# Optimization experiments

Measured on AMD Instinct MI355X. Metric: run time of the kernel, lower is better.

## Reference

```python
import jax, jax.numpy as jnp
import numpy as np

B, S = 32, 1024
ENC_HID, DEC_HID = 512, 512
NEG = -1e10


def setup_inputs() -> dict:
    key = jax.random.key(0)
    k1, k2, k3, k4, k5, k6 = jax.random.split(key, 6)
    hidden = jax.random.normal(k1, (B, DEC_HID), dtype=jnp.float32)
    encoder_outputs = jax.random.normal(k2, (B, S, 2 * ENC_HID), dtype=jnp.float32)
    mask = jax.random.randint(k3, (B, S), 0, 2, dtype=jnp.int32)
    # Linear(enc_hid*2 + dec_hid -> dec_hid): weight [out, in], bias [out]
    in_dim = 2 * ENC_HID + DEC_HID
    W = jax.random.normal(k4, (DEC_HID, in_dim), dtype=jnp.float32) * (1.0 / np.sqrt(in_dim))
    b = jax.random.normal(k5, (DEC_HID,), dtype=jnp.float32) * 0.01
    v = jax.random.uniform(k6, (DEC_HID,), dtype=jnp.float32)  # torch.rand
    return {"hidden": hidden, "encoder_outputs": encoder_outputs, "mask": mask,
            "W": W, "b": b, "v": v}


def reference(hidden, encoder_outputs, mask, W, b, v):
    # cat((hidden_repeated, encoder_outputs)) @ W.T == hidden @ Wh.T + enc @ We.T
    # split W by the concat order: first DEC_HID input cols act on hidden.
    Wh = W[:, :DEC_HID]          # [dec_hid, dec_hid]
    We = W[:, DEC_HID:]          # [dec_hid, 2*enc_hid]
    h_proj = hidden @ Wh.T + b                       # [B, dec_hid]
    e_proj = jnp.einsum('bse,de->bsd', encoder_outputs, We)  # [B, S, dec_hid]
    energy = jnp.tanh(h_proj[:, None, :] + e_proj)   # [B, S, dec_hid]
    scores = energy @ v                               # [B, S]
    scores = jnp.where(mask == 0, NEG, scores)
    return jax.nn.softmax(scores, axis=1)
```

## Files before the change

kernel.cpp:

```cpp
#include <hip/hip_runtime.h>
#include <hip/hip_bf16.h>
#include <math.h>

#define BB 32
#define SS 1024
#define DH 512
#define EH2 1024
#define WROW 1536
#define NEGV -1.0e10f

typedef __attribute__((ext_vector_type(8))) short s16x8;
typedef __attribute__((ext_vector_type(4))) float f32x4;
typedef unsigned short u16;
typedef unsigned int u32;

__device__ __forceinline__ int swzB(int row, int slot) {
    return row * 64 + ((slot ^ (row & 7)) << 3);
}
__device__ __forceinline__ int swzA(int row, int slot) {
    return row * 32 + ((slot ^ ((row >> 1) & 3)) << 3);
}

__device__ __forceinline__ void split8(const float4& v0, const float4& v1,
                                       s16x8& hi, s16x8& lo) {
    float xs[8] = {v0.x, v0.y, v0.z, v0.w, v1.x, v1.y, v1.z, v1.w};
    union { u16 u[8]; s16x8 v; } H, L;
#pragma unroll
    for (int j = 0; j < 8; ++j) {
        u32 u = __builtin_bit_cast(u32, xs[j]);
        u32 hb = u & 0xFFFF0000u;
        float rem = xs[j] - __builtin_bit_cast(float, hb);
        H.u[j] = (u16)(u >> 16);
        L.u[j] = __builtin_bit_cast(u16, __float2bfloat16(rem));
    }
    hi = H.v;
    lo = L.v;
}

__device__ __forceinline__ s16x8 cvt8(const float4& v0, const float4& v1) {
    float xs[8] = {v0.x, v0.y, v0.z, v0.w, v1.x, v1.y, v1.z, v1.w};
    union { u16 u[8]; s16x8 v; } H;
#pragma unroll
    for (int j = 0; j < 8; ++j)
        H.u[j] = __builtin_bit_cast(u16, __float2bfloat16(xs[j]));
    return H.v;
}

__device__ __forceinline__ float fast_tanh(float x) {
    float a = fabsf(x);
    float e = __expf(2.0f * a);
    float r = 1.0f - 2.0f / (e + 1.0f);
    return copysignf(r, x);
}

__global__ void hproj_kernel(const float* __restrict__ hidden,
                             const float* __restrict__ W,
                             const float* __restrict__ bias,
                             float* __restrict__ hproj) {
    int wave = (int)((blockIdx.x * blockDim.x + threadIdx.x) >> 6);
    int lane = threadIdx.x & 63;
    if (wave >= BB * DH) return;
    int b = wave >> 9;
    int d = wave & 511;
    const float* hrow = hidden + b * DH;
    const float* wrow = W + (size_t)d * WROW;
    float sum = 0.f;
#pragma unroll
    for (int u = 0; u < 8; ++u) {
        int k = lane + 64 * u;
        sum = fmaf(hrow[k], wrow[k], sum);
    }
#pragma unroll
    for (int off = 32; off > 0; off >>= 1)
        sum += __shfl_xor(sum, off, 64);
    if (lane == 0) hproj[wave] = sum + bias[d];
}

__global__ void bsplit_kernel(const float* __restrict__ W,
                              u16* __restrict__ img) {
    int idx = blockIdx.x * 256 + threadIdx.x;
    int c = idx >> 7;
    int ko = idx & 127;
    int k = ko * 8;
    const float* src = W + (size_t)c * WROW + DH + k;
    float4 v0 = *(const float4*)src;
    float4 v1 = *(const float4*)(src + 4);
    s16x8 hi, lo;
    split8(v0, v1, hi, lo);
    int nb = c >> 8;
    int cp = c & 255;
    int kt = ko >> 2;
    int sl = ko & 3;
    u16* tb = img + ((size_t)(nb * 32 + kt) << 14);
    *(s16x8*)(tb + swzB(cp, sl)) = hi;
    *(s16x8*)(tb + swzB(cp, sl + 4)) = lo;
}

__global__ __launch_bounds__(512, 4)
void energy_mfma_kernel(const float* __restrict__ enc,
                        const u16* __restrict__ bimg,
                        const float* __restrict__ hproj,
                        const float* __restrict__ v,
                        float* __restrict__ scoresP) {
    __shared__ u16 sA[2][128 * 32];
    __shared__ u16 sB[2][256 * 64];

    const int tid = threadIdx.x;
    const int lane = tid & 63;
    const int wid = tid >> 6;
    const int lr = lane & 15;
    const int lg = lane >> 4;

    const int flat = (blockIdx.x & 7) * 64 + (blockIdx.x >> 3);
    const int nblk = flat & 1;
    const int mblk = flat >> 1;
    const int b = mblk >> 3;
    const int srow = (mblk & 7) * 128;
    const int d0 = nblk * 256;

    const int wm = (wid >> 2) * 64;
    const int wn = (wid & 3) * 64;

    const float* aBase = enc + ((size_t)(b * SS + srow)) * EH2;
    const u16* tBase = bimg + (((size_t)nblk * 32) << 14);

    const int arow = tid >> 2;
    const int ak8 = tid & 3;

    f32x4 acc[4][4];
#pragma unroll
    for (int m = 0; m < 4; ++m)
#pragma unroll
        for (int n = 0; n < 4; ++n) acc[m][n] = (f32x4){0.f, 0.f, 0.f, 0.f};

    float4 rA[2];
    auto loadA = [&](int t) {
        const float* p = aBase + (size_t)arow * EH2 + t * 32 + ak8 * 8;
        rA[0] = ((const float4*)p)[0];
        rA[1] = ((const float4*)p)[1];
    };
    auto writeA = [&](int buf) {
        s16x8 hi = cvt8(rA[0], rA[1]);
        *(s16x8*)&sA[buf][swzA(arow, ak8)] = hi;
    };
    auto stageB = [&](int t, int buf) {
        const u16* tb = tBase + ((size_t)t << 14);
#pragma unroll
        for (int q = 0; q < 4; ++q) {
            int o = (wid * 4 + q) * 512;
            __builtin_amdgcn_global_load_lds(
                (const __attribute__((address_space(1))) u32*)(tb + o + lane * 8),
                (__attribute__((address_space(3))) u32*)&sB[buf][o],
                16, 0, 0);
        }
    };

    auto compute = [&](int buf) {
        s16x8 bH[4], bL[4];
#pragma unroll
        for (int n = 0; n < 4; ++n) {
            int col = wn + n * 16 + lr;
            bH[n] = *(const s16x8*)&sB[buf][swzB(col, lg)];
            bL[n] = *(const s16x8*)&sB[buf][swzB(col, lg + 4)];
        }
        __builtin_amdgcn_s_setprio(1);
#pragma unroll
        for (int m = 0; m < 4; ++m) {
            int row = wm + m * 16 + lr;
            s16x8 aH = *(const s16x8*)&sA[buf][swzA(row, lg)];
#pragma unroll
            for (int n = 0; n < 4; ++n) {
                acc[m][n] = __builtin_amdgcn_mfma_f32_16x16x32_bf16(aH, bH[n], acc[m][n], 0, 0, 0);
                acc[m][n] = __builtin_amdgcn_mfma_f32_16x16x32_bf16(aH, bL[n], acc[m][n], 0, 0, 0);
            }
        }
        __builtin_amdgcn_s_setprio(0);
    };

    loadA(0);
    stageB(0, 0);
    writeA(0);
    loadA(1);
    asm volatile("s_waitcnt vmcnt(2) lgkmcnt(0)" ::: "memory");
    __builtin_amdgcn_s_barrier();

#pragma unroll 1
    for (int t = 0; t < 32; ++t) {
        const int cur = t & 1;
        __builtin_amdgcn_sched_barrier(0);
        if (t < 31) {
            stageB(t + 1, cur ^ 1);
            writeA(cur ^ 1);
            if (t < 30) loadA(t + 2);
        }
        compute(cur);
        if (t < 30) {
            asm volatile("s_waitcnt vmcnt(2) lgkmcnt(0)" ::: "memory");
        } else {
            asm volatile("s_waitcnt vmcnt(0) lgkmcnt(0)" ::: "memory");
        }
        __builtin_amdgcn_s_barrier();
    }

    float* sred = (float*)&sA[0][0];
    float hp[4], vv[4];
#pragma unroll
    for (int n = 0; n < 4; ++n) {
        int c = d0 + wn + n * 16 + lr;
        hp[n] = hproj[b * DH + c];
        vv[n] = v[c];
    }
#pragma unroll
    for (int m = 0; m < 4; ++m)
#pragma unroll
        for (int r = 0; r < 4; ++r) {
            float p = 0.f;
#pragma unroll
            for (int n = 0; n < 4; ++n)
                p += fast_tanh(acc[m][n][r] + hp[n]) * vv[n];
            p += __shfl_xor(p, 1, 64);
            p += __shfl_xor(p, 2, 64);
            p += __shfl_xor(p, 4, 64);
            p += __shfl_xor(p, 8, 64);
            if (lr == 0)
                sred[(wid & 3) * 128 + wm + m * 16 + lg * 4 + r] = p;
        }
    __syncthreads();
    if (tid < 128) {
        float s = sred[0 * 128 + tid] + sred[1 * 128 + tid]
                + sred[2 * 128 + tid] + sred[3 * 128 + tid];
        scoresP[(size_t)nblk * BB * SS + b * SS + srow + tid] = s;
    }
}

__global__ void softmax_kernel(const float* __restrict__ scoresP,
                               const int* __restrict__ mask,
                               float* __restrict__ out) {
    __shared__ float red[8];
    int b = blockIdx.x;
    int tid = threadIdx.x;
    int lane = tid & 63;
    int wid = tid >> 6;

    float x[4];
    float mx = -INFINITY;
#pragma unroll
    for (int u = 0; u < 4; ++u) {
        int s = tid + 256 * u;
        float sc = scoresP[b * SS + s] + scoresP[BB * SS + b * SS + s];
        if (mask[b * SS + s] == 0) sc = NEGV;
        x[u] = sc;
        mx = fmaxf(mx, sc);
    }
#pragma unroll
    for (int off = 32; off > 0; off >>= 1)
        mx = fmaxf(mx, __shfl_xor(mx, off, 64));
    if (lane == 0) red[wid] = mx;
    __syncthreads();
    mx = fmaxf(fmaxf(red[0], red[1]), fmaxf(red[2], red[3]));

    float sum = 0.f;
#pragma unroll
    for (int u = 0; u < 4; ++u) {
        x[u] = expf(x[u] - mx);
        sum += x[u];
    }
#pragma unroll
    for (int off = 32; off > 0; off >>= 1)
        sum += __shfl_xor(sum, off, 64);
    __syncthreads();
    if (lane == 0) red[4 + wid] = sum;
    __syncthreads();
    sum = red[4] + red[5] + red[6] + red[7];
    float inv = 1.0f / sum;
#pragma unroll
    for (int u = 0; u < 4; ++u)
        out[b * SS + tid + 256 * u] = x[u] * inv;
}

extern "C" void kernel_launch(void* const* d_in, const int* in_sizes, int n_in,
                              void* d_out, int out_size, void* d_ws, size_t ws_size,
                              hipStream_t stream) {
    const float* hidden = (const float*)d_in[0];
    const float* enc    = (const float*)d_in[1];
    const int*   mask   = (const int*)d_in[2];
    const float* W      = (const float*)d_in[3];
    const float* bias   = (const float*)d_in[4];
    const float* v      = (const float*)d_in[5];
    float* out = (float*)d_out;

    float* hproj = (float*)d_ws;
    float* scoresP = (float*)((char*)d_ws + 64 * 1024);
    u16* bimg = (u16*)((char*)d_ws + 320 * 1024);

    bsplit_kernel<<<256, 256, 0, stream>>>(W, bimg);
    hproj_kernel<<<BB * DH / 4, 256, 0, stream>>>(hidden, W, bias, hproj);
    energy_mfma_kernel<<<512, 512, 0, stream>>>(enc, bimg, hproj, v, scoresP);
    softmax_kernel<<<BB, 256, 0, stream>>>(scoresP, mask, out);
}
```

Baseline: 82.84 us.

## Load B fragments directly into registers from a fragment-ordered image, drop LDS B staging

```diff
diff --git a/kernel.cpp b/kernel.cpp
--- a/kernel.cpp
+++ b/kernel.cpp
@@ -14,9 +14,6 @@
 typedef unsigned short u16;
 typedef unsigned int u32;
 
-__device__ __forceinline__ int swzB(int row, int slot) {
-    return row * 64 + ((slot ^ (row & 7)) << 3);
-}
 __device__ __forceinline__ int swzA(int row, int slot) {
     return row * 32 + ((slot ^ ((row >> 1) & 3)) << 3);
 }
@@ -89,21 +86,25 @@
     split8(v0, v1, hi, lo);
     int nb = c >> 8;
     int cp = c & 255;
+    int wv = cp >> 6;
+    int n = (cp >> 4) & 3;
+    int lr2 = cp & 15;
     int kt = ko >> 2;
-    int sl = ko & 3;
-    u16* tb = img + ((size_t)(nb * 32 + kt) << 14);
-    *(s16x8*)(tb + swzB(cp, sl)) = hi;
-    *(s16x8*)(tb + swzB(cp, sl + 4)) = lo;
-}
-
-__global__ __launch_bounds__(512, 4)
+    int lg2 = ko & 3;
+    int lane2 = lg2 * 16 + lr2;
+    size_t base = (size_t)nb * 524288 + (size_t)kt * 16384
+                + wv * 4096 + (n * 2) * 512 + lane2 * 8;
+    *(s16x8*)(img + base) = hi;
+    *(s16x8*)(img + base + 512) = lo;
+}
+
+__global__ __launch_bounds__(256, 3)
 void energy_mfma_kernel(const float* __restrict__ enc,
                         const u16* __restrict__ bimg,
                         const float* __restrict__ hproj,
                         const float* __restrict__ v,
                         float* __restrict__ scoresP) {
-    __shared__ u16 sA[2][128 * 32];
-    __shared__ u16 sB[2][256 * 64];
+    __shared__ u16 sA[2][64 * 32];
 
     const int tid = threadIdx.x;
     const int lane = tid & 63;
@@ -111,18 +112,16 @@
     const int lr = lane & 15;
     const int lg = lane >> 4;
 
-    const int flat = (blockIdx.x & 7) * 64 + (blockIdx.x >> 3);
+    const int flat = (blockIdx.x & 7) * 128 + (blockIdx.x >> 3);
     const int nblk = flat & 1;
     const int mblk = flat >> 1;
-    const int b = mblk >> 3;
-    const int srow = (mblk & 7) * 128;
+    const int b = mblk >> 4;
+    const int srow = (mblk & 15) * 64;
     const int d0 = nblk * 256;
-
-    const int wm = (wid >> 2) * 64;
-    const int wn = (wid & 3) * 64;
+    const int wn = wid * 64;
 
     const float* aBase = enc + ((size_t)(b * SS + srow)) * EH2;
-    const u16* tBase = bimg + (((size_t)nblk * 32) << 14);
+    const u16* fBase = bimg + (size_t)nblk * 524288 + wid * 4096 + lane * 8;
 
     const int arow = tid >> 2;
     const int ak8 = tid & 3;
@@ -143,62 +142,55 @@
         s16x8 hi = cvt8(rA[0], rA[1]);
         *(s16x8*)&sA[buf][swzA(arow, ak8)] = hi;
     };
-    auto stageB = [&](int t, int buf) {
-        const u16* tb = tBase + ((size_t)t << 14);
-#pragma unroll
-        for (int q = 0; q < 4; ++q) {
-            int o = (wid * 4 + q) * 512;
-            __builtin_amdgcn_global_load_lds(
-                (const __attribute__((address_space(1))) u32*)(tb + o + lane * 8),
-                (__attribute__((address_space(3))) u32*)&sB[buf][o],
-                16, 0, 0);
-        }
-    };
-
-    auto compute = [&](int buf) {
-        s16x8 bH[4], bL[4];
-#pragma unroll
-        for (int n = 0; n < 4; ++n) {
-            int col = wn + n * 16 + lr;
-            bH[n] = *(const s16x8*)&sB[buf][swzB(col, lg)];
-            bL[n] = *(const s16x8*)&sB[buf][swzB(col, lg + 4)];
-        }
-        __builtin_amdgcn_s_setprio(1);
+    auto loadBF = [&](int t, s16x8* F) {
+        const u16* p = fBase + (size_t)t * 16384;
+#pragma unroll
+        for (int j = 0; j < 8; ++j)
+            F[j] = *(const s16x8*)(p + j * 512);
+    };
+    auto compute = [&](int buf, s16x8* F) {
 #pragma unroll
         for (int m = 0; m < 4; ++m) {
-            int row = wm + m * 16 + lr;
-            s16x8 aH = *(const s16x8*)&sA[buf][swzA(row, lg)];
+            s16x8 aH = *(const s16x8*)&sA[buf][swzA(m * 16 + lr, lg)];
 #pragma unroll
             for (int n = 0; n < 4; ++n) {
-                acc[m][n] = __builtin_amdgcn_mfma_f32_16x16x32_bf16(aH, bH[n], acc[m][n], 0, 0, 0);
-                acc[m][n] = __builtin_amdgcn_mfma_f32_16x16x32_bf16(aH, bL[n], acc[m][n], 0, 0, 0);
+                acc[m][n] = __builtin_amdgcn_mfma_f32_16x16x32_bf16(aH, F[n * 2], acc[m][n], 0, 0, 0);
+                acc[m][n] = __builtin_amdgcn_mfma_f32_16x16x32_bf16(aH, F[n * 2 + 1], acc[m][n], 0, 0, 0);
             }
         }
-        __builtin_amdgcn_s_setprio(0);
-    };
-
+    };
+
+    s16x8 F0[8], F1[8];
     loadA(0);
-    stageB(0, 0);
+    loadBF(0, F0);
     writeA(0);
     loadA(1);
-    asm volatile("s_waitcnt vmcnt(2) lgkmcnt(0)" ::: "memory");
+    loadBF(1, F1);
+    asm volatile("s_waitcnt lgkmcnt(0)" ::: "memory");
     __builtin_amdgcn_s_barrier();
 
 #pragma unroll 1
-    for (int t = 0; t < 32; ++t) {
-        const int cur = t & 1;
+    for (int tt = 0; tt < 16; ++tt) {
+        const int t = 2 * tt;
         __builtin_amdgcn_sched_barrier(0);
-        if (t < 31) {
-            stageB(t + 1, cur ^ 1);
-            writeA(cur ^ 1);
-            if (t < 30) loadA(t + 2);
-        }
-        compute(cur);
-        if (t < 30) {
-            asm volatile("s_waitcnt vmcnt(2) lgkmcnt(0)" ::: "memory");
-        } else {
-            asm volatile("s_waitcnt vmcnt(0) lgkmcnt(0)" ::: "memory");
-        }
+        compute(0, F0);
+        writeA(1);
+        if (t + 2 < 32) {
+            loadA(t + 2);
+            loadBF(t + 2, F0);
+        }
+        asm volatile("s_waitcnt lgkmcnt(0)" ::: "memory");
+        __builtin_amdgcn_s_barrier();
+        __builtin_amdgcn_sched_barrier(0);
+        compute(1, F1);
+        if (t + 2 < 32) {
+            writeA(0);
+            if (t + 3 < 32) {
+                loadA(t + 3);
+                loadBF(t + 3, F1);
+            }
+        }
+        asm volatile("s_waitcnt lgkmcnt(0)" ::: "memory");
         __builtin_amdgcn_s_barrier();
     }
 
@@ -223,12 +215,12 @@
             p += __shfl_xor(p, 4, 64);
             p += __shfl_xor(p, 8, 64);
             if (lr == 0)
-                sred[(wid & 3) * 128 + wm + m * 16 + lg * 4 + r] = p;
-        }
-    __syncthreads();
-    if (tid < 128) {
-        float s = sred[0 * 128 + tid] + sred[1 * 128 + tid]
-                + sred[2 * 128 + tid] + sred[3 * 128 + tid];
+                sred[wid * 64 + m * 16 + lg * 4 + r] = p;
+        }
+    __syncthreads();
+    if (tid < 64) {
+        float s = sred[0 * 64 + tid] + sred[1 * 64 + tid]
+                + sred[2 * 64 + tid] + sred[3 * 64 + tid];
         scoresP[(size_t)nblk * BB * SS + b * SS + srow + tid] = s;
     }
 }
@@ -295,6 +287,6 @@
 
     bsplit_kernel<<<256, 256, 0, stream>>>(W, bimg);
     hproj_kernel<<<BB * DH / 4, 256, 0, stream>>>(hidden, W, bias, hproj);
-    energy_mfma_kernel<<<512, 512, 0, stream>>>(enc, bimg, hproj, v, scoresP);
+    energy_mfma_kernel<<<1024, 256, 0, stream>>>(enc, bimg, hproj, v, scoresP);
     softmax_kernel<<<BB, 256, 0, stream>>>(scoresP, mask, out);
 }
```

New measurement: 91.23 us. +10.1%, slower.
